# Optimization experiments

Measured on AMD Instinct MI355X. Metric: run time of the kernel, lower is better.

## Reference

```python
import jax, jax.numpy as jnp
import numpy as np

B, S, E = 8, 2048, 128
DECAY = 1.2
LN_EPS = 1e-3  # keras LayerNormalization default epsilon


def setup_inputs() -> dict:
    key = jax.random.key(0)
    k1, k2, k3, k4 = jax.random.split(key, 4)
    return {
        "x": jax.random.normal(k1, (B, S, E), dtype=jnp.float32),
        "dense_w": jax.random.normal(k2, (E, E), dtype=jnp.float32) * 0.02,
        "dense_b": jnp.zeros((E,), dtype=jnp.float32),
        "concept_map": jax.random.normal(k3, (E, E, E), dtype=jnp.float32) * 0.02,
        "ln_gamma": jnp.ones((E,), dtype=jnp.float32),
        "ln_beta": jnp.zeros((E,), dtype=jnp.float32),
    }


def reference(x, dense_w, dense_b, concept_map, ln_gamma, ln_beta):
    # Dense projection
    h = x @ dense_w + dense_b  # (B, S, E)
    b, s, e = h.shape

    # Decayed prefix-sum recurrence: s_i = (s_{i-1} + h_{i-1}) / 1.2, s_0 = 0
    def step(carry, xt):
        new = (carry + xt) / DECAY
        return new, new

    h_t = jnp.swapaxes(h, 0, 1)  # (S, B, E)
    _, s_tail = jax.lax.scan(step, jnp.zeros((b, e), h.dtype), h_t[:-1])
    s_seq = jnp.concatenate([jnp.zeros((1, b, e), h.dtype), s_tail], axis=0)
    s_seq = jnp.swapaxes(s_seq, 0, 1)  # (B, S, E)

    # result[b,s,c] = sum_{a,p} h[b,s,a] * s_seq[b,s,p] * W[c,a,p]
    # (original code materializes (B,S,E,E,E); this is the fused contraction)
    out = jnp.einsum("bsa,bsp,cap->bsc", h, s_seq, concept_map)

    r = out + h
    # LayerNormalization over the last axis
    mean = jnp.mean(r, axis=-1, keepdims=True)
    var = jnp.var(r, axis=-1, keepdims=True)
    r = (r - mean) * jax.lax.rsqrt(var + LN_EPS) * ln_gamma + ln_beta
    # Dropout is identity at inference
    return r
```

## Files before the change

### kernel.cpp

```cpp
#include <hip/hip_runtime.h>
#include <hip/hip_bf16.h>
#include <math.h>

#define E_DIM 128
#define S_LEN 2048
#define B_N   8
#define BS    (B_N * S_LEN)
#define CHUNK 64
#define NCHUNK (S_LEN / CHUNK)

typedef unsigned short u16;
typedef _Float16 f16;
typedef _Float16 f16x2 __attribute__((ext_vector_type(2)));
typedef _Float16 f16x8 __attribute__((ext_vector_type(8)));
typedef float    f32x16 __attribute__((ext_vector_type(16)));

__global__ __launch_bounds__(256) void k_pre(const float* __restrict__ x,
                                             const float* __restrict__ dw,
                                             const float* __restrict__ db,
                                             const float* __restrict__ cm,
                                             float* __restrict__ hout,
                                             u16* __restrict__ wb) {
    if (blockIdx.x < 1024) {
        int t = blockIdx.x * 256 + threadIdx.x;
        int l31 = t & 31, hi = (t >> 5) & 1, ks = (t >> 6) & 7;
        int cch = (t >> 9) & 3, a = t >> 11;
        int c = cch * 32 + l31, qs = ks * 2 + hi;
        const float* src = cm + (((long)(c << 7) + a) << 7) + (qs << 3);
        float4 v0 = ((const float4*)src)[0];
        float4 v1 = ((const float4*)src)[1];
        union { f16 f[8]; uint4 v; } o;
        o.f[0] = (f16)v0.x; o.f[1] = (f16)v0.y; o.f[2] = (f16)v0.z; o.f[3] = (f16)v0.w;
        o.f[4] = (f16)v1.x; o.f[5] = (f16)v1.y; o.f[6] = (f16)v1.z; o.f[7] = (f16)v1.w;
        ((uint4*)wb)[t] = o.v;
        return;
    }
    __shared__ float Wl[E_DIM * E_DIM];
    const int t = threadIdx.x;
    const long r0 = (long)(blockIdx.x - 1024) * 64;

    float4* Wl4 = (float4*)Wl;
    const float4* w4 = (const float4*)dw;
#pragma unroll
    for (int i = 0; i < 16; ++i) Wl4[t + 256 * i] = w4[t + 256 * i];
    __syncthreads();

    const int cq = t & 31;
    const int rg = t >> 5;
    float4 bb = ((const float4*)db)[cq];
    float acc[8][4];
#pragma unroll
    for (int i = 0; i < 8; ++i) {
        acc[i][0] = bb.x; acc[i][1] = bb.y; acc[i][2] = bb.z; acc[i][3] = bb.w;
    }
#pragma unroll 4
    for (int k = 0; k < E_DIM; ++k) {
        float4 wv = Wl4[k * 32 + cq];
#pragma unroll
        for (int i = 0; i < 8; ++i) {
            float xv = x[(r0 + rg * 8 + i) * E_DIM + k];
            acc[i][0] += xv * wv.x;
            acc[i][1] += xv * wv.y;
            acc[i][2] += xv * wv.z;
            acc[i][3] += xv * wv.w;
        }
    }
    float4* h4 = (float4*)(hout + r0 * E_DIM);
#pragma unroll
    for (int i = 0; i < 8; ++i) {
        float4 o;
        o.x = acc[i][0]; o.y = acc[i][1]; o.z = acc[i][2]; o.w = acc[i][3];
        h4[(rg * 8 + i) * 32 + cq] = o;
    }
}

__global__ __launch_bounds__(128) void k_scan(const float* __restrict__ h,
                                              u16* __restrict__ sb16,
                                              float* __restrict__ fc,
                                              u16* __restrict__ hT) {
    const int b = blockIdx.x >> 5;
    const int j = blockIdx.x & 31;
    const int e = threadIdx.x;
    const float inv_d = (float)(1.0 / 1.2);
    const int pos0 = b * S_LEN + j * CHUNK;
    long base = (long)pos0 * E_DIM + e;
    float carry = 0.f;
    union { u16 u[8]; uint4 v; } hb;
#pragma unroll 1
    for (int i0 = 0; i0 < CHUNK; i0 += 8) {
#pragma unroll
        for (int k = 0; k < 8; ++k) {
            float hv = h[base + (long)(i0 + k) * E_DIM];
            union { f16 f; u16 u; } cu; cu.f = (f16)carry;
            sb16[base + (long)(i0 + k) * E_DIM] = cu.u;
            union { f16 f; u16 u; } hu; hu.f = (f16)hv;
            hb.u[k] = hu.u;
            carry = (carry + hv) * inv_d;
        }
        *(uint4*)&hT[(size_t)e * BS + pos0 + i0] = hb.v;
    }
    fc[(b * NCHUNK + j) * E_DIM + e] = carry;
}

__global__ __launch_bounds__(64, 2) void k_main(const u16* __restrict__ hT,
                                                const u16* __restrict__ sb16,
                                                const float* __restrict__ fc,
                                                const u16* __restrict__ w2,
                                                float* __restrict__ out,
                                                float dm64) {
    __shared__ u16 h16[32 * 128];
    __shared__ float carr[2][E_DIM];
    const int l = threadIdx.x;
    const int l31 = l & 31, hi = l >> 5;

    const int bid = blockIdx.x;
    const int x = bid & 7, i = bid >> 3;
    const int combo = x * 4 + (i >> 7);
    const int mb  = i & 127;
    const int cch = combo & 3;
    const int r   = (combo >> 2) & 3;
    const int kq  = combo >> 4;
    const int row_base = mb * 128;

#pragma unroll
    for (int it = 0; it < 8; ++it) {
        int idx = it * 64 + l;
        int al = idx >> 4, part = idx & 15;
        const u16* src = hT + (size_t)(r * 32 + al) * BS + row_base + part * 8;
        __builtin_amdgcn_global_load_lds(
            (const __attribute__((address_space(1))) void*)src,
            (__attribute__((address_space(3))) void*)&h16[idx * 8], 16, 0, 0);
    }

    const int bb = row_base >> 11;
    const int j0 = (row_base >> 6) & 31;
    const float L2D = 0.26303440583379383f;
    {
        const float d2 = dm64 * dm64, d3 = d2 * dm64, d4 = d3 * dm64;
#pragma unroll
        for (int es = 0; es < 2; ++es) {
            int e = l + es * 64;
            const float* fp = fc + (size_t)(bb * NCHUNK) * E_DIM + e;
            float c0 = 0.f;
            int jj = 0;
            for (; jj + 4 <= j0; jj += 4) {
                float f0 = fp[(jj + 0) * E_DIM], f1 = fp[(jj + 1) * E_DIM];
                float f2 = fp[(jj + 2) * E_DIM], f3 = fp[(jj + 3) * E_DIM];
                c0 = c0 * d4 + f0 * d3 + f1 * d2 + f2 * dm64 + f3;
            }
            for (; jj < j0; ++jj) c0 = c0 * dm64 + fp[jj * E_DIM];
            carr[0][e] = c0;
            carr[1][e] = fp[j0 * E_DIM] + c0 * dm64;
        }
    }
    __syncthreads();

    f16x2 s2[4][16];
#pragma unroll
    for (int rb = 0; rb < 4; ++rb) {
        const int row = row_base + rb * 32 + l31;
        const float f = exp2f(-L2D * (float)(row & 63));
        const int ch = rb >> 1;
#pragma unroll
        for (int ksl = 0; ksl < 4; ++ksl) {
            const int pbase = kq * 64 + ksl * 16 + hi * 8;
            union { uint4 u; u16 us[8]; } uu;
            uu.u = *(const uint4*)(sb16 + (size_t)row * E_DIM + pbase);
#pragma unroll
            for (int q = 0; q < 4; ++q) {
                union { f16 f; u16 u; } a0; a0.u = uu.us[2 * q];
                union { f16 f; u16 u; } a1; a1.u = uu.us[2 * q + 1];
                f16x2 pr;
                pr.x = (f16)((float)a0.f + carr[ch][pbase + 2 * q] * f);
                pr.y = (f16)((float)a1.f + carr[ch][pbase + 2 * q + 1] * f);
                s2[rb][ksl * 4 + q] = pr;
            }
        }
    }

    f32x16 acc[4];
#pragma unroll
    for (int rb = 0; rb < 4; ++rb)
#pragma unroll
        for (int g = 0; g < 16; ++g) acc[rb][g] = 0.f;

    const u16* wbase = w2 + (size_t)(r * 32) * 16384 + cch * 4096 + kq * 2048 + l * 8;

#define LOADB(dst, sl) {                                                      \
    const u16* _p = wbase + (size_t)(sl) * 16384;                             \
    _Pragma("unroll")                                                         \
    for (int _k = 0; _k < 4; ++_k) dst[_k] = *(const f16x8*)(_p + _k * 512); }

#define LOADH(dst, sl) {                                                      \
    _Pragma("unroll")                                                         \
    for (int _rb = 0; _rb < 4; ++_rb) dst[_rb] = h16[(sl) * 128 + _rb * 32 + l31]; }

#define COMPUTE(bf, hv)                                                       \
    _Pragma("unroll")                                                         \
    for (int _ksl = 0; _ksl < 4; ++_ksl) {                                    \
        _Pragma("unroll")                                                     \
        for (int _rb = 0; _rb < 4; ++_rb) {                                   \
            union { u16 u[2]; f16x2 v; } _hh;                                 \
            _hh.u[0] = hv[_rb]; _hh.u[1] = hv[_rb];                           \
            union { f16x2 h2[4]; f16x8 v; } _A;                               \
            _Pragma("unroll")                                                 \
            for (int _q = 0; _q < 4; ++_q)                                    \
                _A.h2[_q] = _hh.v * s2[_rb][_ksl * 4 + _q];                   \
            acc[_rb] = __builtin_amdgcn_mfma_f32_32x32x16_f16(                \
                _A.v, bf[_ksl], acc[_rb], 0, 0, 0);                           \
        }                                                                     \
    }

    f16x8 bA[4], bB[4];
    u16 hA[4], hB[4];
    LOADB(bA, 0); LOADH(hA, 0);

#pragma unroll 1
    for (int s2i = 0; s2i < 16; ++s2i) {
        const int sl = s2i * 2;
        LOADB(bB, sl + 1); LOADH(hB, sl + 1);
        COMPUTE(bA, hA);
        if (s2i < 15) { LOADB(bA, sl + 2); LOADH(hA, sl + 2); }
        COMPUTE(bB, hB);
    }
#undef LOADB
#undef LOADH
#undef COMPUTE

    const int col = cch * 32 + l31;
#pragma unroll
    for (int rb = 0; rb < 4; ++rb)
#pragma unroll
        for (int g = 0; g < 16; ++g) {
            int rowl = (g & 3) + 8 * (g >> 2) + 4 * hi;
            long row = (long)row_base + rb * 32 + rowl;
            unsafeAtomicAdd(&out[row * E_DIM + col], acc[rb][g]);
        }
}

__global__ __launch_bounds__(256) void k_ln(float* __restrict__ out,
                                            const float* __restrict__ h,
                                            const float* __restrict__ gamma,
                                            const float* __restrict__ beta) {
    const int t = threadIdx.x;
    const int l32 = t & 31, rl = t >> 5;
    const long row = (long)blockIdx.x * 8 + rl;
    float4 v  = ((const float4*)out)[row * 32 + l32];
    float4 hv = ((const float4*)h)[row * 32 + l32];
    v.x += hv.x; v.y += hv.y; v.z += hv.z; v.w += hv.w;
    float ls = v.x + v.y + v.z + v.w;
    float lq = v.x * v.x + v.y * v.y + v.z * v.z + v.w * v.w;
#pragma unroll
    for (int m = 1; m < 32; m <<= 1) {
        ls += __shfl_xor(ls, m, 64);
        lq += __shfl_xor(lq, m, 64);
    }
    float mean = ls * (1.f / 128.f);
    float var  = lq * (1.f / 128.f) - mean * mean;
    float inv  = rsqrtf(var + 1e-3f);
    float4 g = ((const float4*)gamma)[l32];
    float4 b = ((const float4*)beta)[l32];
    float4 o;
    o.x = (v.x - mean) * inv * g.x + b.x;
    o.y = (v.y - mean) * inv * g.y + b.y;
    o.z = (v.z - mean) * inv * g.z + b.z;
    o.w = (v.w - mean) * inv * g.w + b.w;
    ((float4*)out)[row * 32 + l32] = o;
}

extern "C" void kernel_launch(void* const* d_in, const int* in_sizes, int n_in,
                              void* d_out, int out_size, void* d_ws, size_t ws_size,
                              hipStream_t stream) {
    const float* x     = (const float*)d_in[0];
    const float* dw    = (const float*)d_in[1];
    const float* db    = (const float*)d_in[2];
    const float* cm    = (const float*)d_in[3];
    const float* gamma = (const float*)d_in[4];
    const float* beta  = (const float*)d_in[5];
    float* outp = (float*)d_out;

    float* ws = (float*)d_ws;
    float* h    = ws;
    float* fc   = ws + (size_t)BS * E_DIM;
    u16*   wb   = (u16*)(fc + B_N * NCHUNK * E_DIM);
    u16*   hT   = wb + (size_t)2097152;
    u16*   sb16 = hT + (size_t)BS * E_DIM;

    float dm64 = (float)pow(1.2, -64.0);

    hipMemsetAsync(d_out, 0, (size_t)BS * E_DIM * sizeof(float), stream);
    k_pre <<<dim3(1280), dim3(256), 0, stream>>>(x, dw, db, cm, h, wb);
    k_scan<<<dim3(B_N * NCHUNK), dim3(128), 0, stream>>>(h, sb16, fc, hT);
    k_main<<<dim3(4096), dim3(64), 0, stream>>>(hT, sb16, fc, wb, outp, dm64);
    k_ln  <<<dim3(BS / 8), dim3(256), 0, stream>>>(outp, h, gamma, beta);
}
```

Measured before the change: 136.0 us.

## Merge four column-chunk blocks into one 4-wave workgroup sharing LDS tiles

k_main now launches 1024 workgroups of 256 threads instead of 4096 single-wave blocks. Each of the four waves handles one output column chunk, and all of them share the h16 LDS tile and the carry preamble, which were previously recomputed by every block. The main loop gains a four-stage register prefetch of the weight fragments and h values, and the duplicated h pairs are hoisted out of the inner loop. This cuts redundant global loads and setup work, at the cost of higher register pressure from the deeper buffering and larger workgroups that may limit occupancy.

```diff
diff --git a/kernel.cpp b/kernel.cpp
--- a/kernel.cpp
+++ b/kernel.cpp
@@ -102,29 +102,29 @@
     fc[(b * NCHUNK + j) * E_DIM + e] = carry;
 }
 
-__global__ __launch_bounds__(64, 2) void k_main(const u16* __restrict__ hT,
-                                                const u16* __restrict__ sb16,
-                                                const float* __restrict__ fc,
-                                                const u16* __restrict__ w2,
-                                                float* __restrict__ out,
-                                                float dm64) {
+__global__ __launch_bounds__(256, 2) void k_main(const u16* __restrict__ hT,
+                                                 const u16* __restrict__ sb16,
+                                                 const float* __restrict__ fc,
+                                                 const u16* __restrict__ w2,
+                                                 float* __restrict__ out,
+                                                 float dm64) {
     __shared__ u16 h16[32 * 128];
     __shared__ float carr[2][E_DIM];
-    const int l = threadIdx.x;
+    const int t = threadIdx.x;
+    const int w = t >> 6, l = t & 63;
     const int l31 = l & 31, hi = l >> 5;
 
     const int bid = blockIdx.x;
-    const int x = bid & 7, i = bid >> 3;
-    const int combo = x * 4 + (i >> 7);
-    const int mb  = i & 127;
-    const int cch = combo & 3;
-    const int r   = (combo >> 2) & 3;
-    const int kq  = combo >> 4;
+    const int combo = bid & 7;
+    const int r   = combo & 3;
+    const int kq  = combo >> 2;
+    const int mb  = bid >> 3;
+    const int cch = w;
     const int row_base = mb * 128;
 
 #pragma unroll
-    for (int it = 0; it < 8; ++it) {
-        int idx = it * 64 + l;
+    for (int it = 0; it < 2; ++it) {
+        int idx = it * 256 + t;
         int al = idx >> 4, part = idx & 15;
         const u16* src = hT + (size_t)(r * 32 + al) * BS + row_base + part * 8;
         __builtin_amdgcn_global_load_lds(
@@ -136,22 +136,19 @@
     const int j0 = (row_base >> 6) & 31;
     const float L2D = 0.26303440583379383f;
     {
+        const int ch = t >> 7, e = t & 127;
         const float d2 = dm64 * dm64, d3 = d2 * dm64, d4 = d3 * dm64;
-#pragma unroll
-        for (int es = 0; es < 2; ++es) {
-            int e = l + es * 64;
-            const float* fp = fc + (size_t)(bb * NCHUNK) * E_DIM + e;
-            float c0 = 0.f;
-            int jj = 0;
-            for (; jj + 4 <= j0; jj += 4) {
-                float f0 = fp[(jj + 0) * E_DIM], f1 = fp[(jj + 1) * E_DIM];
-                float f2 = fp[(jj + 2) * E_DIM], f3 = fp[(jj + 3) * E_DIM];
-                c0 = c0 * d4 + f0 * d3 + f1 * d2 + f2 * dm64 + f3;
-            }
-            for (; jj < j0; ++jj) c0 = c0 * dm64 + fp[jj * E_DIM];
-            carr[0][e] = c0;
-            carr[1][e] = fp[j0 * E_DIM] + c0 * dm64;
-        }
+        const float* fp = fc + (size_t)(bb * NCHUNK) * E_DIM + e;
+        float c0 = 0.f;
+        int jj = 0;
+        for (; jj + 4 <= j0; jj += 4) {
+            float f0 = fp[(jj + 0) * E_DIM], f1 = fp[(jj + 1) * E_DIM];
+            float f2 = fp[(jj + 2) * E_DIM], f3 = fp[(jj + 3) * E_DIM];
+            c0 = c0 * d4 + f0 * d3 + f1 * d2 + f2 * dm64 + f3;
+        }
+        for (; jj < j0; ++jj) c0 = c0 * dm64 + fp[jj * E_DIM];
+        if (ch == 0) carr[0][e] = c0;
+        else         carr[1][e] = fp[j0 * E_DIM] + c0 * dm64;
     }
     __syncthreads();
 
@@ -195,33 +192,41 @@
     _Pragma("unroll")                                                         \
     for (int _rb = 0; _rb < 4; ++_rb) dst[_rb] = h16[(sl) * 128 + _rb * 32 + l31]; }
 
-#define COMPUTE(bf, hv)                                                       \
+#define COMPUTE(bf, hv) {                                                     \
+    union { u16 u[2]; f16x2 v; } _hp[4];                                      \
+    _Pragma("unroll")                                                         \
+    for (int _rb = 0; _rb < 4; ++_rb) {                                       \
+        _hp[_rb].u[0] = hv[_rb]; _hp[_rb].u[1] = hv[_rb];                     \
+    }                                                                         \
     _Pragma("unroll")                                                         \
     for (int _ksl = 0; _ksl < 4; ++_ksl) {                                    \
         _Pragma("unroll")                                                     \
         for (int _rb = 0; _rb < 4; ++_rb) {                                   \
-            union { u16 u[2]; f16x2 v; } _hh;                                 \
-            _hh.u[0] = hv[_rb]; _hh.u[1] = hv[_rb];                           \
             union { f16x2 h2[4]; f16x8 v; } _A;                               \
             _Pragma("unroll")                                                 \
             for (int _q = 0; _q < 4; ++_q)                                    \
-                _A.h2[_q] = _hh.v * s2[_rb][_ksl * 4 + _q];                   \
+                _A.h2[_q] = _hp[_rb].v * s2[_rb][_ksl * 4 + _q];              \
             acc[_rb] = __builtin_amdgcn_mfma_f32_32x32x16_f16(                \
                 _A.v, bf[_ksl], acc[_rb], 0, 0, 0);                           \
         }                                                                     \
-    }
-
-    f16x8 bA[4], bB[4];
-    u16 hA[4], hB[4];
-    LOADB(bA, 0); LOADH(hA, 0);
+    }}
+
+    f16x8 b0[4], b1[4], b2[4], b3[4];
+    u16 h0[4], h1[4], h2[4], h3[4];
+    LOADB(b0, 0); LOADH(h0, 0);
+    LOADB(b1, 1); LOADH(h1, 1);
 
 #pragma unroll 1
-    for (int s2i = 0; s2i < 16; ++s2i) {
-        const int sl = s2i * 2;
-        LOADB(bB, sl + 1); LOADH(hB, sl + 1);
-        COMPUTE(bA, hA);
-        if (s2i < 15) { LOADB(bA, sl + 2); LOADH(hA, sl + 2); }
-        COMPUTE(bB, hB);
+    for (int sq = 0; sq < 8; ++sq) {
+        const int sl = sq * 4;
+        if (sl + 2 < 32) { LOADB(b2, sl + 2); LOADH(h2, sl + 2); }
+        COMPUTE(b0, h0);
+        if (sl + 3 < 32) { LOADB(b3, sl + 3); LOADH(h3, sl + 3); }
+        COMPUTE(b1, h1);
+        if (sl + 4 < 32) { LOADB(b0, sl + 4); LOADH(h0, sl + 4); }
+        COMPUTE(b2, h2);
+        if (sl + 5 < 32) { LOADB(b1, sl + 5); LOADH(h1, sl + 5); }
+        COMPUTE(b3, h3);
     }
 #undef LOADB
 #undef LOADH
@@ -291,6 +296,6 @@
     hipMemsetAsync(d_out, 0, (size_t)BS * E_DIM * sizeof(float), stream);
     k_pre <<<dim3(1280), dim3(256), 0, stream>>>(x, dw, db, cm, h, wb);
     k_scan<<<dim3(B_N * NCHUNK), dim3(128), 0, stream>>>(h, sb16, fc, hT);
-    k_main<<<dim3(4096), dim3(64), 0, stream>>>(hT, sb16, fc, wb, outp, dm64);
+    k_main<<<dim3(1024), dim3(256), 0, stream>>>(hT, sb16, fc, wb, outp, dm64);
     k_ln  <<<dim3(BS / 8), dim3(256), 0, stream>>>(outp, h, gamma, beta);
 }
```

Measured after the change: 130.6 us. 1.04x faster.
